# Kernel optimization log

Hardware: AMD Instinct MI355X
Metric: run time of the kernel (lower is better)

The kernel has to match this reference:

```python
import jax, jax.numpy as jnp
import numpy as np

# pywt 'haar': dec_lo = [1/sqrt2, 1/sqrt2], dec_hi = [-1/sqrt2, 1/sqrt2]
_SQ = np.float32(1.0 / np.sqrt(2.0))
_DEC_LO = np.array([_SQ, _SQ], dtype=np.float32)
_DEC_HI = np.array([-_SQ, _SQ], dtype=np.float32)


def _make_filter():
    ll = np.outer(_DEC_LO, _DEC_LO)
    lh = np.outer(_DEC_HI, _DEC_LO)
    hl = np.outer(_DEC_LO, _DEC_HI)
    hh = np.outer(_DEC_HI, _DEC_HI)
    # torch code writes filters flipped ([::-1, ::-1]) then uses cross-correlation
    f = np.stack([ll, lh, hl, hh], axis=0)[:, ::-1, ::-1]  # [4, 2, 2]
    return jnp.asarray(np.ascontiguousarray(f))


def setup_inputs() -> dict:
    key = jax.random.key(0)
    x = jax.random.normal(key, (8, 64, 256, 256), dtype=jnp.float32)
    return {"x": x}


def reference(x):
    B, C, H, W = x.shape
    filt = _make_filter()  # [4, 2, 2]
    # The torch module's split/pad/conv3d/split/cat pipeline is equivalent to a
    # depthwise 2x2 conv producing 4 subbands per channel, ordered
    # [c0:(LL,LH,HL,HH), c1:(LL,LH,HL,HH), ...] along the channel dim.
    kernel = jnp.tile(filt[None], (C, 1, 1, 1)).reshape(C * 4, 1, 2, 2)
    # F.pad(..., (0,1,0,1)): pad right and bottom by 1 with zeros
    xp = jnp.pad(x, ((0, 0), (0, 0), (0, 1), (0, 1)))
    out = jax.lax.conv_general_dilated(
        xp, kernel,
        window_strides=(1, 1),
        padding='VALID',
        dimension_numbers=('NCHW', 'OIHW', 'NCHW'),
        feature_group_count=C,
    )
    return out  # [B, 4*C, H, W]
```

## Files before the change

### kernel.cpp

```cpp
#include <hip/hip_runtime.h>


constexpr int Bn = 8, Cn = 64, Hn = 256, Wn = 256;
constexpr int ROWS_PER_BLOCK = 4;

__global__ __launch_bounds__(256)
void haar_dwt_kernel(const float* __restrict__ x, float* __restrict__ out) {
    const int tid  = threadIdx.x;
    const int lane = tid & 63;
    const int rib  = tid >> 6;

    const int rows_groups = Hn / ROWS_PER_BLOCK;
    const int rg  = blockIdx.x % rows_groups;
    const int bc  = blockIdx.x / rows_groups;
    const int row = rg * ROWS_PER_BLOCK + rib;
    const int j0  = lane * 4;

    const size_t plane_elems = (size_t)Hn * Wn;
    const float* plane = x + (size_t)bc * plane_elems;

    const float* p0 = plane + (size_t)row * Wn + j0;
    float4 r0 = *reinterpret_cast<const float4*>(p0);
    float  e0 = (j0 + 4 < Wn) ? p0[4] : 0.0f;

    float4 r1 = make_float4(0.f, 0.f, 0.f, 0.f);
    float  e1 = 0.0f;
    if (row + 1 < Hn) {
        const float* p1 = p0 + Wn;
        r1 = *reinterpret_cast<const float4*>(p1);
        e1 = (j0 + 4 < Wn) ? p1[4] : 0.0f;
    }

    float a0[5] = {r0.x, r0.y, r0.z, r0.w, e0};
    float a1[5] = {r1.x, r1.y, r1.z, r1.w, e1};

    float4 vll, vlh, vhl, vhh;
    float* pll = reinterpret_cast<float*>(&vll);
    float* plh = reinterpret_cast<float*>(&vlh);
    float* phl = reinterpret_cast<float*>(&vhl);
    float* phh = reinterpret_cast<float*>(&vhh);

#pragma unroll
    for (int k = 0; k < 4; ++k) {
        const float x00 = a0[k], x01 = a0[k + 1];
        const float x10 = a1[k], x11 = a1[k + 1];
        const float sum0 = x00 + x01;
        const float dif0 = x00 - x01;
        const float sum1 = x10 + x11;
        const float dif1 = x10 - x11;
        pll[k] = 0.5f * (sum0 + sum1);
        plh[k] = 0.5f * (sum0 - sum1);
        phl[k] = 0.5f * (dif0 + dif1);
        phh[k] = 0.5f * (dif0 - dif1);
    }

    const int b = bc / Cn;
    const int c = bc % Cn;
    float* obase = out + ((size_t)(b * 4 * Cn + 4 * c)) * plane_elems
                       + (size_t)row * Wn + j0;

    *reinterpret_cast<float4*>(obase)                   = vll;
    *reinterpret_cast<float4*>(obase + plane_elems)     = vlh;
    *reinterpret_cast<float4*>(obase + 2 * plane_elems) = vhl;
    *reinterpret_cast<float4*>(obase + 3 * plane_elems) = vhh;
}

extern "C" void kernel_launch(void* const* d_in, const int* in_sizes, int n_in,
                              void* d_out, int out_size, void* d_ws, size_t ws_size,
                              hipStream_t stream) {
    const float* x = (const float*)d_in[0];
    float* out = (float*)d_out;

    const int grid = Bn * Cn * (Hn / ROWS_PER_BLOCK);
    haar_dwt_kernel<<<grid, 256, 0, stream>>>(x, out);
}
```

Measured before the change: 597.7 us.

## Process four rows per wave with shared halo rows and nontemporal stores

Each wave now computes four consecutive output rows, loading five input rows so the neighbor row is reused instead of re-read by another wave. Output subbands are written with nontemporal stores to avoid polluting cache with streaming writes, and the grid becomes 2D to drop div/mod index math. Fewer blocks and more registers per thread may reduce latency hiding.

```diff
diff --git a/kernel.cpp b/kernel.cpp
--- a/kernel.cpp
+++ b/kernel.cpp
@@ -1,68 +1,75 @@
 #include <hip/hip_runtime.h>
 
 
+typedef float f32x4 __attribute__((ext_vector_type(4)));
+
 constexpr int Bn = 8, Cn = 64, Hn = 256, Wn = 256;
-constexpr int ROWS_PER_BLOCK = 4;
+constexpr int ROWS_PER_WAVE   = 4;
+constexpr int WAVES_PER_BLOCK = 4;
+constexpr int ROWS_PER_BLOCK  = ROWS_PER_WAVE * WAVES_PER_BLOCK;
 
 __global__ __launch_bounds__(256)
 void haar_dwt_kernel(const float* __restrict__ x, float* __restrict__ out) {
     const int tid  = threadIdx.x;
     const int lane = tid & 63;
-    const int rib  = tid >> 6;
+    const int wv   = tid >> 6;
 
-    const int rows_groups = Hn / ROWS_PER_BLOCK;
-    const int rg  = blockIdx.x % rows_groups;
-    const int bc  = blockIdx.x / rows_groups;
-    const int row = rg * ROWS_PER_BLOCK + rib;
-    const int j0  = lane * 4;
+    const int bc   = blockIdx.y;
+    const int row0 = blockIdx.x * ROWS_PER_BLOCK + wv * ROWS_PER_WAVE;
+    const int j0   = lane * 4;
 
     const size_t plane_elems = (size_t)Hn * Wn;
-    const float* plane = x + (size_t)bc * plane_elems;
+    const float* p = x + (size_t)bc * plane_elems + (size_t)row0 * Wn + j0;
 
-    const float* p0 = plane + (size_t)row * Wn + j0;
-    float4 r0 = *reinterpret_cast<const float4*>(p0);
-    float  e0 = (j0 + 4 < Wn) ? p0[4] : 0.0f;
+    f32x4 r[ROWS_PER_WAVE + 1];
+    float e[ROWS_PER_WAVE + 1];
+    const bool has_e = (j0 + 4 < Wn);
 
-    float4 r1 = make_float4(0.f, 0.f, 0.f, 0.f);
-    float  e1 = 0.0f;
-    if (row + 1 < Hn) {
-        const float* p1 = p0 + Wn;
-        r1 = *reinterpret_cast<const float4*>(p1);
-        e1 = (j0 + 4 < Wn) ? p1[4] : 0.0f;
+#pragma unroll
+    for (int k = 0; k < ROWS_PER_WAVE; ++k) {
+        const float* pk = p + k * Wn;
+        r[k] = *reinterpret_cast<const f32x4*>(pk);
+        e[k] = has_e ? pk[4] : 0.0f;
+    }
+    {
+        const f32x4 zero4 = {0.f, 0.f, 0.f, 0.f};
+        f32x4 rl = zero4;
+        float el = 0.0f;
+        if (row0 + ROWS_PER_WAVE < Hn) {
+            const float* pk = p + ROWS_PER_WAVE * Wn;
+            rl = *reinterpret_cast<const f32x4*>(pk);
+            el = has_e ? pk[4] : 0.0f;
+        }
+        r[ROWS_PER_WAVE] = rl;
+        e[ROWS_PER_WAVE] = el;
     }
 
-    float a0[5] = {r0.x, r0.y, r0.z, r0.w, e0};
-    float a1[5] = {r1.x, r1.y, r1.z, r1.w, e1};
-
-    float4 vll, vlh, vhl, vhh;
-    float* pll = reinterpret_cast<float*>(&vll);
-    float* plh = reinterpret_cast<float*>(&vlh);
-    float* phl = reinterpret_cast<float*>(&vhl);
-    float* phh = reinterpret_cast<float*>(&vhh);
+    float* obase = out + (size_t)(4 * bc) * plane_elems + (size_t)row0 * Wn + j0;
 
 #pragma unroll
-    for (int k = 0; k < 4; ++k) {
-        const float x00 = a0[k], x01 = a0[k + 1];
-        const float x10 = a1[k], x11 = a1[k + 1];
-        const float sum0 = x00 + x01;
-        const float dif0 = x00 - x01;
-        const float sum1 = x10 + x11;
-        const float dif1 = x10 - x11;
-        pll[k] = 0.5f * (sum0 + sum1);
-        plh[k] = 0.5f * (sum0 - sum1);
-        phl[k] = 0.5f * (dif0 + dif1);
-        phh[k] = 0.5f * (dif0 - dif1);
+    for (int i = 0; i < ROWS_PER_WAVE; ++i) {
+        const float a0[5] = {r[i][0], r[i][1], r[i][2], r[i][3], e[i]};
+        const float a1[5] = {r[i+1][0], r[i+1][1], r[i+1][2], r[i+1][3], e[i+1]};
+
+        f32x4 vll, vlh, vhl, vhh;
+#pragma unroll
+        for (int k = 0; k < 4; ++k) {
+            const float sum0 = a0[k] + a0[k + 1];
+            const float dif0 = a0[k] - a0[k + 1];
+            const float sum1 = a1[k] + a1[k + 1];
+            const float dif1 = a1[k] - a1[k + 1];
+            vll[k] = 0.5f * (sum0 + sum1);
+            vlh[k] = 0.5f * (sum0 - sum1);
+            vhl[k] = 0.5f * (dif0 + dif1);
+            vhh[k] = 0.5f * (dif0 - dif1);
+        }
+
+        float* orow = obase + i * Wn;
+        __builtin_nontemporal_store(vll, reinterpret_cast<f32x4*>(orow));
+        __builtin_nontemporal_store(vlh, reinterpret_cast<f32x4*>(orow + plane_elems));
+        __builtin_nontemporal_store(vhl, reinterpret_cast<f32x4*>(orow + 2 * plane_elems));
+        __builtin_nontemporal_store(vhh, reinterpret_cast<f32x4*>(orow + 3 * plane_elems));
     }
-
-    const int b = bc / Cn;
-    const int c = bc % Cn;
-    float* obase = out + ((size_t)(b * 4 * Cn + 4 * c)) * plane_elems
-                       + (size_t)row * Wn + j0;
-
-    *reinterpret_cast<float4*>(obase)                   = vll;
-    *reinterpret_cast<float4*>(obase + plane_elems)     = vlh;
-    *reinterpret_cast<float4*>(obase + 2 * plane_elems) = vhl;
-    *reinterpret_cast<float4*>(obase + 3 * plane_elems) = vhh;
 }
 
 extern "C" void kernel_launch(void* const* d_in, const int* in_sizes, int n_in,
@@ -71,6 +78,6 @@
     const float* x = (const float*)d_in[0];
     float* out = (float*)d_out;
 
-    const int grid = Bn * Cn * (Hn / ROWS_PER_BLOCK);
+    dim3 grid(Hn / ROWS_PER_BLOCK, Bn * Cn);
     haar_dwt_kernel<<<grid, 256, 0, stream>>>(x, out);
 }
```

Result: slower. 616.3 us (+3.1%).
